# Performance work log

Measured on AMD Instinct MI355X. Metric: run time of the kernel, lower is better.

Reference implementation:

```python
import jax, jax.numpy as jnp
import numpy as np

N = 4096        # n_nodes
IN = 512        # in_features
HEADS = 8       # n_heads
HID = 64        # n_hidden = out_features // n_heads
SLOPE = 0.2     # leaky relu negative slope


def setup_inputs() -> dict:
    key = jax.random.key(0)
    k1, k2, k3, k4 = jax.random.split(key, 4)
    h = jax.random.normal(k1, (N, IN), dtype=jnp.float32)
    W = jax.random.normal(k2, (IN, HEADS * HID), dtype=jnp.float32) * 0.05
    a = jax.random.normal(k3, (2 * HID,), dtype=jnp.float32) * 0.05
    adj = jax.random.uniform(k4, (N, N)) < 0.01
    adj = adj | jnp.eye(N, dtype=bool)
    return {"h": h, "adj_mat": adj[..., None], "W": W, "a": a}


def reference(h, adj_mat, W, a):
    # g[i, h, f] = per-head projected features
    g = (h @ W).reshape(N, HEADS, HID)
    # attention Linear on concat([g_i, g_j]) splits into two dot products
    a_l, a_r = a[:HID], a[HID:]
    el = jnp.einsum('ihf,f->ih', g, a_l)   # score contribution of target i
    er = jnp.einsum('jhf,f->jh', g, a_r)   # score contribution of source j
    e = el[:, None, :] + er[None, :, :]    # [N, N, HEADS]
    e = jnp.where(e >= 0, e, SLOPE * e)    # LeakyReLU
    e = jnp.where(adj_mat, e, -jnp.inf)    # mask non-edges (adj broadcasts over heads)
    attn = jax.nn.softmax(e, axis=1)       # softmax over source nodes j
    out = jnp.einsum('ijh,jhf->ihf', attn, g)
    return out.reshape(N, HEADS * HID)     # is_concat=True
```

## Files before the change

### kernel.cpp

```cpp
#include <hip/hip_runtime.h>
#include <cstdint>
#include <cstddef>

#define N_NODES 4096
#define IN_DIM  512
#define HEADS   8
#define HID     64
#define OUTF    (HEADS * HID)
#define SLOPE   0.2f
#define MAXD    256
#define MAXD2   128

typedef __bf16 bf16_t;
typedef __attribute__((ext_vector_type(8))) __bf16 bf16x8;
typedef __attribute__((ext_vector_type(4))) float    f32x4;

#define GLD16(gp, lp)                                                                  \
    __builtin_amdgcn_global_load_lds((const __attribute__((address_space(1))) void*)(gp), \
                                     (__attribute__((address_space(3))) void*)(lp), 16, 0, 0)

__device__ __forceinline__ unsigned short to_bf16_u(float x) {
    uint32_t u = __builtin_bit_cast(uint32_t, x);
    u += 0x7fffu + ((u >> 16) & 1u);
    return (unsigned short)(u >> 16);
}
__device__ __forceinline__ float bfbits_to_f(unsigned short b) {
    uint32_t u = ((uint32_t)b) << 16;
    return __builtin_bit_cast(float, u);
}

__global__ __launch_bounds__(256) void prep_conv(const float* __restrict__ h,
                                                 unsigned short* __restrict__ hhi,
                                                 const float* __restrict__ W,
                                                 unsigned short* __restrict__ whiT,
                                                 unsigned short* __restrict__ wloT) {
    const int b = blockIdx.x;
    const int tid = threadIdx.x;
    if (b < 2048) {
        const int t = b * 256 + tid;
        const float4 v = ((const float4*)h)[t];
        ushort4 hi;
        hi.x = to_bf16_u(v.x); hi.y = to_bf16_u(v.y);
        hi.z = to_bf16_u(v.z); hi.w = to_bf16_u(v.w);
        ((ushort4*)hhi)[t] = hi;
    } else {
        const int idx = (b - 2048) * 256 + tid;
        const int c   = idx & 511;
        const int kq  = (idx >> 9) * 4;
        ushort4 hv, lv;
        float w0 = W[(size_t)(kq + 0) * OUTF + c];
        float w1 = W[(size_t)(kq + 1) * OUTF + c];
        float w2 = W[(size_t)(kq + 2) * OUTF + c];
        float w3 = W[(size_t)(kq + 3) * OUTF + c];
        hv.x = to_bf16_u(w0); lv.x = to_bf16_u(w0 - bfbits_to_f(hv.x));
        hv.y = to_bf16_u(w1); lv.y = to_bf16_u(w1 - bfbits_to_f(hv.y));
        hv.z = to_bf16_u(w2); lv.z = to_bf16_u(w2 - bfbits_to_f(hv.z));
        hv.w = to_bf16_u(w3); lv.w = to_bf16_u(w3 - bfbits_to_f(hv.w));
        *(ushort4*)&whiT[(size_t)c * IN_DIM + kq] = hv;
        *(ushort4*)&wloT[(size_t)c * IN_DIM + kq] = lv;
    }
}

__global__ __launch_bounds__(256) void gemm_pack(const bf16_t* __restrict__ Ahi,
                                                 const bf16_t* __restrict__ BhiT,
                                                 const bf16_t* __restrict__ BloT,
                                                 const float* __restrict__ a,
                                                 unsigned short* __restrict__ Gb,
                                                 float* __restrict__ el,
                                                 float* __restrict__ er,
                                                 const int* __restrict__ adj,
                                                 unsigned short* __restrict__ bm16) {
    __shared__ bf16_t As[2][64 * 32];
    __shared__ bf16_t Bh[2][64 * 32];
    __shared__ bf16_t Bl[2][64 * 32];
    __shared__ float  elp[2][64], erp[2][64];

    const int tid = threadIdx.x;

    if (blockIdx.x >= 512) {
        const int t = (blockIdx.x - 512) * 256 + tid;
        const int4* src = (const int4*)adj + (size_t)t * 4;
        const int4 v0 = src[0], v1 = src[1], v2 = src[2], v3 = src[3];
        uint32_t m = 0;
        m |= (v0.x != 0) ? 1u << 0 : 0;  m |= (v0.y != 0) ? 1u << 1 : 0;
        m |= (v0.z != 0) ? 1u << 2 : 0;  m |= (v0.w != 0) ? 1u << 3 : 0;
        m |= (v1.x != 0) ? 1u << 4 : 0;  m |= (v1.y != 0) ? 1u << 5 : 0;
        m |= (v1.z != 0) ? 1u << 6 : 0;  m |= (v1.w != 0) ? 1u << 7 : 0;
        m |= (v2.x != 0) ? 1u << 8 : 0;  m |= (v2.y != 0) ? 1u << 9 : 0;
        m |= (v2.z != 0) ? 1u << 10 : 0; m |= (v2.w != 0) ? 1u << 11 : 0;
        m |= (v3.x != 0) ? 1u << 12 : 0; m |= (v3.y != 0) ? 1u << 13 : 0;
        m |= (v3.z != 0) ? 1u << 14 : 0; m |= (v3.w != 0) ? 1u << 15 : 0;
        bm16[t] = (unsigned short)m;
        return;
    }

    const int wid = tid >> 6;
    const int lane = tid & 63;
    const int head = blockIdx.x & 7;
    const int i0 = (blockIdx.x >> 3) * 64;
    const int j0 = head * 64;
    const int l15 = lane & 15, kq = lane >> 4;

    const int srow = tid >> 2;
    const int sc   = (tid & 3) ^ ((srow >> 1) & 3);
    const size_t aoff = (size_t)(i0 + srow) * IN_DIM + sc * 8;
    const size_t boff = (size_t)(j0 + srow) * IN_DIM + sc * 8;

    const int wm = wid >> 1, wn = wid & 1;
    int aro[2], bro[2];
#pragma unroll
    for (int m = 0; m < 2; ++m) {
        const int row = wm * 32 + m * 16 + l15;
        aro[m] = row * 32 + (kq ^ ((row >> 1) & 3)) * 8;
    }
#pragma unroll
    for (int n = 0; n < 2; ++n) {
        const int col = wn * 32 + n * 16 + l15;
        bro[n] = col * 32 + (kq ^ ((col >> 1) & 3)) * 8;
    }

    f32x4 acc[2][2] = {};

    auto stage = [&](int buf, int t) {
        const size_t k0 = (size_t)t * 32;
        GLD16(Ahi  + aoff + k0, &As[buf][tid * 8]);
        GLD16(BhiT + boff + k0, &Bh[buf][tid * 8]);
        GLD16(BloT + boff + k0, &Bl[buf][tid * 8]);
    };

    stage(0, 0);
    for (int t = 0; t < 16; ++t) {
        const int cur = t & 1;
        if (t < 15) {
            stage(cur ^ 1, t + 1);
            asm volatile("s_waitcnt vmcnt(3)" ::: "memory");
        } else {
            asm volatile("s_waitcnt vmcnt(0)" ::: "memory");
        }
        __builtin_amdgcn_s_barrier();
        asm volatile("" ::: "memory");

        bf16x8 af[2], bhf[2], blf[2];
#pragma unroll
        for (int m = 0; m < 2; ++m) af[m] = *(const bf16x8*)&As[cur][aro[m]];
#pragma unroll
        for (int n = 0; n < 2; ++n) bhf[n] = *(const bf16x8*)&Bh[cur][bro[n]];
#pragma unroll
        for (int n = 0; n < 2; ++n) blf[n] = *(const bf16x8*)&Bl[cur][bro[n]];
#pragma unroll
        for (int m = 0; m < 2; ++m)
#pragma unroll
            for (int n = 0; n < 2; ++n) {
                acc[m][n] = __builtin_amdgcn_mfma_f32_16x16x32_bf16(af[m], bhf[n], acc[m][n], 0, 0, 0);
                acc[m][n] = __builtin_amdgcn_mfma_f32_16x16x32_bf16(af[m], blf[n], acc[m][n], 0, 0, 0);
            }

        __builtin_amdgcn_s_barrier();
        asm volatile("" ::: "memory");
    }

#pragma unroll
    for (int m = 0; m < 2; ++m)
#pragma unroll
        for (int n = 0; n < 2; ++n) {
            const int col = j0 + wn * 32 + n * 16 + l15;
#pragma unroll
            for (int q = 0; q < 4; ++q) {
                const int row = i0 + wm * 32 + m * 16 + kq * 4 + q;
                Gb[(size_t)row * OUTF + col] = to_bf16_u(acc[m][n][q]);
            }
        }

    float al[2], arr[2];
#pragma unroll
    for (int n = 0; n < 2; ++n) {
        al[n]  = a[wn * 32 + n * 16 + l15];
        arr[n] = a[64 + wn * 32 + n * 16 + l15];
    }
#pragma unroll
    for (int m = 0; m < 2; ++m)
#pragma unroll
        for (int q = 0; q < 4; ++q) {
            float pe = 0.f, pr = 0.f;
#pragma unroll
            for (int n = 0; n < 2; ++n) {
                const float v = acc[m][n][q];
                pe = fmaf(v, al[n], pe);
                pr = fmaf(v, arr[n], pr);
            }
#pragma unroll
            for (int off = 1; off < 16; off <<= 1) {
                pe += __shfl_xor(pe, off);
                pr += __shfl_xor(pr, off);
            }
            if (l15 == 0) {
                const int lrow = wm * 32 + m * 16 + kq * 4 + q;
                elp[wn][lrow] = pe;
                erp[wn][lrow] = pr;
            }
        }
    __syncthreads();
    if (tid < 64) {
        el[(size_t)(i0 + tid) * HEADS + head] = elp[0][tid] + elp[1][tid];
        er[(size_t)(i0 + tid) * HEADS + head] = erp[0][tid] + erp[1][tid];
    }
}

__global__ __launch_bounds__(512) void gat_attn_wave(const unsigned long long* __restrict__ bm64,
                                                     const unsigned short* __restrict__ Gb,
                                                     const float* __restrict__ el,
                                                     const float* __restrict__ er,
                                                     float* __restrict__ out) {
    __shared__ float pw[8][8][MAXD2 + 8];
    __shared__ int   nbr[8][MAXD2];
    const int tid = threadIdx.x;
    const int lane = tid & 63;
    const int wid = tid >> 6;
    const int i = blockIdx.x * 8 + wid;

    unsigned long long q = bm64[(size_t)i * 64 + lane];
    const int c = __popcll(q);
    int inc = c;
#pragma unroll
    for (int off = 1; off < 64; off <<= 1) {
        const int t = __shfl_up(inc, off);
        if (lane >= off) inc += t;
    }
    const int deg = min(__shfl(inc, 63), MAXD2);
    int pos = inc - c;
    while (q) {
        const int b = __builtin_ctzll(q);
        q &= q - 1;
        if (pos < MAXD2) nbr[wid][pos] = lane * 64 + b;
        ++pos;
    }
    asm volatile("s_waitcnt lgkmcnt(0)" ::: "memory");
    __builtin_amdgcn_wave_barrier();

    const float4 el_lo = *(const float4*)(el + (size_t)i * 8);
    const float4 el_hi = *(const float4*)(el + (size_t)i * 8 + 4);
    float mx[8];
#pragma unroll
    for (int h = 0; h < 8; ++h) mx[h] = -1e30f;
    for (int j = lane; j < deg; j += 64) {
        const int nj = nbr[wid][j];
        const float4 er_lo = *(const float4*)(er + (size_t)nj * 8);
        const float4 er_hi = *(const float4*)(er + (size_t)nj * 8 + 4);
        float e[8] = {el_lo.x + er_lo.x, el_lo.y + er_lo.y, el_lo.z + er_lo.z, el_lo.w + er_lo.w,
                      el_hi.x + er_hi.x, el_hi.y + er_hi.y, el_hi.z + er_hi.z, el_hi.w + er_hi.w};
#pragma unroll
        for (int h = 0; h < 8; ++h) {
            e[h] = (e[h] >= 0.f) ? e[h] : SLOPE * e[h];
            pw[wid][h][j] = e[h];
            mx[h] = fmaxf(mx[h], e[h]);
        }
    }
#pragma unroll
    for (int off = 1; off < 64; off <<= 1)
#pragma unroll
        for (int h = 0; h < 8; ++h) mx[h] = fmaxf(mx[h], __shfl_xor(mx[h], off));

    float s8[8] = {};
    for (int j = lane; j < deg; j += 64) {
#pragma unroll
        for (int h = 0; h < 8; ++h) {
            const float pe = __expf(pw[wid][h][j] - mx[h]);
            pw[wid][h][j] = pe;
            s8[h] += pe;
        }
    }
#pragma unroll
    for (int off = 1; off < 64; off <<= 1)
#pragma unroll
        for (int h = 0; h < 8; ++h) s8[h] += __shfl_xor(s8[h], off);
    asm volatile("s_waitcnt lgkmcnt(0)" ::: "memory");
    __builtin_amdgcn_wave_barrier();

    const int myhead = lane >> 3;
    float sv = s8[0];
    sv = (myhead == 1) ? s8[1] : sv;
    sv = (myhead == 2) ? s8[2] : sv;
    sv = (myhead == 3) ? s8[3] : sv;
    sv = (myhead == 4) ? s8[4] : sv;
    sv = (myhead == 5) ? s8[5] : sv;
    sv = (myhead == 6) ? s8[6] : sv;
    sv = (myhead == 7) ? s8[7] : sv;
    const float inv = 1.f / sv;

    float a8[8] = {};
    const unsigned short* gl = Gb + lane * 8;
#pragma unroll 2
    for (int j = 0; j < deg; ++j) {
        const int nj = nbr[wid][j];
        const float w = pw[wid][myhead][j];
        const uint4 v = *(const uint4*)(gl + (size_t)nj * OUTF);
        a8[0] = fmaf(w, bfbits_to_f((unsigned short)(v.x & 0xffffu)), a8[0]);
        a8[1] = fmaf(w, bfbits_to_f((unsigned short)(v.x >> 16)),     a8[1]);
        a8[2] = fmaf(w, bfbits_to_f((unsigned short)(v.y & 0xffffu)), a8[2]);
        a8[3] = fmaf(w, bfbits_to_f((unsigned short)(v.y >> 16)),     a8[3]);
        a8[4] = fmaf(w, bfbits_to_f((unsigned short)(v.z & 0xffffu)), a8[4]);
        a8[5] = fmaf(w, bfbits_to_f((unsigned short)(v.z >> 16)),     a8[5]);
        a8[6] = fmaf(w, bfbits_to_f((unsigned short)(v.w & 0xffffu)), a8[6]);
        a8[7] = fmaf(w, bfbits_to_f((unsigned short)(v.w >> 16)),     a8[7]);
    }
    float4 o0 = {a8[0] * inv, a8[1] * inv, a8[2] * inv, a8[3] * inv};
    float4 o1 = {a8[4] * inv, a8[5] * inv, a8[6] * inv, a8[7] * inv};
    *(float4*)(out + (size_t)i * OUTF + lane * 8)     = o0;
    *(float4*)(out + (size_t)i * OUTF + lane * 8 + 4) = o1;
}

__global__ __launch_bounds__(256) void gemm_f32(const float* __restrict__ A,
                                                const float* __restrict__ B,
                                                float* __restrict__ C) {
    __shared__ float As[16][68];
    __shared__ float Bs[16][64];
    const int tid = threadIdx.x;
    const int tx = tid & 15, ty = tid >> 4;
    const int i0 = blockIdx.y * 64;
    const int j0 = blockIdx.x * 64;
    const int ar = tid >> 2;
    const int ac = (tid & 3) << 2;
    const int bk = tid >> 4;
    const int bc = (tid & 15) << 2;
    float acc[4][4] = {};
    for (int k0 = 0; k0 < IN_DIM; k0 += 16) {
        const float4 av = *(const float4*)(A + (size_t)(i0 + ar) * IN_DIM + k0 + ac);
        const float4 bv = *(const float4*)(B + (size_t)(k0 + bk) * OUTF + j0 + bc);
        __syncthreads();
        As[ac + 0][ar] = av.x; As[ac + 1][ar] = av.y;
        As[ac + 2][ar] = av.z; As[ac + 3][ar] = av.w;
        *(float4*)&Bs[bk][bc] = bv;
        __syncthreads();
#pragma unroll
        for (int k = 0; k < 16; ++k) {
            const float4 a4 = *(const float4*)&As[k][ty << 2];
            const float4 b4 = *(const float4*)&Bs[k][tx << 2];
            const float am[4] = {a4.x, a4.y, a4.z, a4.w};
            const float bn[4] = {b4.x, b4.y, b4.z, b4.w};
#pragma unroll
            for (int m = 0; m < 4; ++m)
#pragma unroll
                for (int n = 0; n < 4; ++n)
                    acc[m][n] = fmaf(am[m], bn[n], acc[m][n]);
        }
    }
#pragma unroll
    for (int m = 0; m < 4; ++m) {
        float4 v = {acc[m][0], acc[m][1], acc[m][2], acc[m][3]};
        *(float4*)(C + (size_t)(i0 + (ty << 2) + m) * OUTF + j0 + (tx << 2)) = v;
    }
}

__global__ __launch_bounds__(512) void el_er_kernel(const float* __restrict__ g,
                                                    const float* __restrict__ a,
                                                    float* __restrict__ el,
                                                    float* __restrict__ er) {
    const int i = blockIdx.x;
    const int wid = threadIdx.x >> 6;
    const int lane = threadIdx.x & 63;
    const float v = g[(size_t)i * OUTF + wid * HID + lane];
    float pl = v * a[lane];
    float pr = v * a[HID + lane];
#pragma unroll
    for (int off = 1; off < 64; off <<= 1) {
        pl += __shfl_xor(pl, off);
        pr += __shfl_xor(pr, off);
    }
    if (lane == 0) {
        el[(size_t)i * HEADS + wid] = pl;
        er[(size_t)i * HEADS + wid] = pr;
    }
}

__global__ __launch_bounds__(512) void gat_attn_f32(const int* __restrict__ adj,
                                                    const float* __restrict__ g,
                                                    const float* __restrict__ el,
                                                    const float* __restrict__ er,
                                                    float* __restrict__ out) {
    const int i = blockIdx.x;
    const int tid = threadIdx.x;
    const int lane = tid & 63;
    const int wid = tid >> 6;

    __shared__ int   nbr[MAXD];
    __shared__ float p[HEADS][MAXD + 2];
    __shared__ float red[8][256];
    __shared__ float sinv[8];
    __shared__ int   wave_base[8];
    __shared__ int   s_deg;

    const int4* row = (const int4*)(adj + (size_t)i * N_NODES);
    const int4 w0 = row[tid * 2 + 0];
    const int4 w1 = row[tid * 2 + 1];
    uint32_t msk = 0;
    if (w0.x) msk |= 1u;   if (w0.y) msk |= 2u;
    if (w0.z) msk |= 4u;   if (w0.w) msk |= 8u;
    if (w1.x) msk |= 16u;  if (w1.y) msk |= 32u;
    if (w1.z) msk |= 64u;  if (w1.w) msk |= 128u;

    const int c = __popc(msk);
    int inc = c;
#pragma unroll
    for (int off = 1; off < 64; off <<= 1) {
        const int t = __shfl_up(inc, off);
        if (lane >= off) inc += t;
    }
    if (lane == 63) wave_base[wid] = inc;
    __syncthreads();
    if (tid == 0) {
        int run = 0;
#pragma unroll
        for (int w = 0; w < 8; ++w) { const int t = wave_base[w]; wave_base[w] = run; run += t; }
        s_deg = run;
    }
    __syncthreads();
    int pos = wave_base[wid] + inc - c;
#pragma unroll
    for (int b = 0; b < 8; ++b) {
        if (msk & (1u << b)) {
            if (pos < MAXD) nbr[pos] = tid * 8 + b;
            ++pos;
        }
    }
    __syncthreads();
    const int deg = min(s_deg, MAXD);

    const float eli = el[(size_t)i * HEADS + wid];
    float m = -1e30f;
    for (int j = lane; j < deg; j += 64) {
        float e = eli + er[(size_t)nbr[j] * HEADS + wid];
        e = (e >= 0.f) ? e : SLOPE * e;
        p[wid][j] = e;
        m = fmaxf(m, e);
    }
#pragma unroll
    for (int off = 1; off < 64; off <<= 1) m = fmaxf(m, __shfl_xor(m, off));
    float s = 0.f;
    for (int j = lane; j < deg; j += 64) {
        const float pe = __expf(p[wid][j] - m);
        p[wid][j] = pe;
        s += pe;
    }
#pragma unroll
    for (int off = 1; off < 64; off <<= 1) s += __shfl_xor(s, off);
    if (lane == 0) sinv[wid] = 1.f / s;
    __syncthreads();

    const int half = wid >> 2, jslot = wid & 3;
    const int head = half * 4 + (lane >> 4);
    const int f4 = (lane & 15) * 4;
    const float* gbase = g + (size_t)head * HID + f4;
    float4 acc = {0.f, 0.f, 0.f, 0.f};
#pragma unroll 4
    for (int j = jslot; j < deg; j += 4) {
        const int nj = nbr[j];
        const float w = p[head][j];
        const float4 v = *(const float4*)(gbase + (size_t)nj * OUTF);
        acc.x = fmaf(w, v.x, acc.x);
        acc.y = fmaf(w, v.y, acc.y);
        acc.z = fmaf(w, v.z, acc.z);
        acc.w = fmaf(w, v.w, acc.w);
    }
    *(float4*)&red[wid][(lane >> 4) * 64 + f4] = acc;
    __syncthreads();

    const int hf = tid >> 8, loc = tid & 255;
    const float v = red[hf * 4 + 0][loc] + red[hf * 4 + 1][loc] +
                    red[hf * 4 + 2][loc] + red[hf * 4 + 3][loc];
    out[(size_t)i * OUTF + tid] = v * sinv[tid >> 6];
}

extern "C" void kernel_launch(void* const* d_in, const int* in_sizes, int n_in,
                              void* d_out, int out_size, void* d_ws, size_t ws_size,
                              hipStream_t stream) {
    const float* h   = (const float*)d_in[0];
    const int*   adj = (const int*)d_in[1];
    const float* W   = (const float*)d_in[2];
    const float* a   = (const float*)d_in[3];
    float* out = (float*)d_out;
    char* ws = (char*)d_ws;

    const size_t G_OFF   = 0;
    const size_t EL_OFF  = 8388608;
    const size_t ER_OFF  = 8519680;
    const size_t BM_OFF  = 8650752;
    const size_t HHI_OFF = 10747904;
    const size_t WHI_OFF = 14942208;
    const size_t WLO_OFF = 15466496;
    const size_t NEED_FULL = 15990784;

    float* el = (float*)(ws + EL_OFF);
    float* er = (float*)(ws + ER_OFF);

    if (ws_size >= NEED_FULL) {
        unsigned short* gbf  = (unsigned short*)(ws + G_OFF);
        unsigned short* bm   = (unsigned short*)(ws + BM_OFF);
        unsigned short* hhi  = (unsigned short*)(ws + HHI_OFF);
        unsigned short* whiT = (unsigned short*)(ws + WHI_OFF);
        unsigned short* wloT = (unsigned short*)(ws + WLO_OFF);
        prep_conv<<<2304, 256, 0, stream>>>(h, hhi, W, whiT, wloT);
        gemm_pack<<<4608, 256, 0, stream>>>((const bf16_t*)hhi, (const bf16_t*)whiT,
                                            (const bf16_t*)wloT, a, gbf, el, er, adj, bm);
        gat_attn_wave<<<512, 512, 0, stream>>>((const unsigned long long*)bm, gbf, el, er, out);
    } else {
        float* g = (float*)(ws + G_OFF);
        gemm_f32<<<dim3(8, 64), 256, 0, stream>>>(h, W, g);
        el_er_kernel<<<N_NODES, 512, 0, stream>>>(g, a, el, er);
        gat_attn_f32<<<N_NODES, 512, 0, stream>>>(adj, g, el, er, out);
    }
}
```

Measured before the change: 49.08 us.

## Split each attention row across two waves and double GEMM K-tile

The GEMM K tile grows from 32 to 64 with a new 8-way XOR swizzle, halving the number of pipeline iterations and barriers. The attention kernel now assigns two waves per node: each computes softmax for four heads and half the neighbour gather, and partial sums are reduced through shared memory before a block-wide store. This doubles the number of waves launched for the latency-bound gather. It costs more LDS per block and adds __syncthreads calls where the old code used only wave-level sync.

```diff
diff --git a/kernel.cpp b/kernel.cpp
--- a/kernel.cpp
+++ b/kernel.cpp
@@ -70,9 +70,9 @@
                                                  float* __restrict__ er,
                                                  const int* __restrict__ adj,
                                                  unsigned short* __restrict__ bm16) {
-    __shared__ bf16_t As[2][64 * 32];
-    __shared__ bf16_t Bh[2][64 * 32];
-    __shared__ bf16_t Bl[2][64 * 32];
+    __shared__ bf16_t As[2][64 * 64];
+    __shared__ bf16_t Bh[2][64 * 64];
+    __shared__ bf16_t Bl[2][64 * 64];
     __shared__ float  elp[2][64], erp[2][64];
 
     const int tid = threadIdx.x;
@@ -101,59 +101,74 @@
     const int j0 = head * 64;
     const int l15 = lane & 15, kq = lane >> 4;
 
-    const int srow = tid >> 2;
-    const int sc   = (tid & 3) ^ ((srow >> 1) & 3);
-    const size_t aoff = (size_t)(i0 + srow) * IN_DIM + sc * 8;
-    const size_t boff = (size_t)(j0 + srow) * IN_DIM + sc * 8;
+    const int sr0 = wid * 16 + (lane >> 3);
+    const int sc  = (lane & 7) ^ (sr0 & 7);
+    const size_t aoff = (size_t)(i0 + sr0) * IN_DIM + sc * 8;
+    const size_t boff = (size_t)(j0 + sr0) * IN_DIM + sc * 8;
+    const int ld0 = wid * 1024 + lane * 8;
 
     const int wm = wid >> 1, wn = wid & 1;
-    int aro[2], bro[2];
+    int aro[2][2], bro[2][2];
 #pragma unroll
     for (int m = 0; m < 2; ++m) {
         const int row = wm * 32 + m * 16 + l15;
-        aro[m] = row * 32 + (kq ^ ((row >> 1) & 3)) * 8;
+#pragma unroll
+        for (int ks = 0; ks < 2; ++ks)
+            aro[m][ks] = row * 64 + (((ks * 4 + kq) ^ (row & 7)) * 8);
     }
 #pragma unroll
     for (int n = 0; n < 2; ++n) {
         const int col = wn * 32 + n * 16 + l15;
-        bro[n] = col * 32 + (kq ^ ((col >> 1) & 3)) * 8;
+#pragma unroll
+        for (int ks = 0; ks < 2; ++ks)
+            bro[n][ks] = col * 64 + (((ks * 4 + kq) ^ (col & 7)) * 8);
     }
 
     f32x4 acc[2][2] = {};
 
     auto stage = [&](int buf, int t) {
-        const size_t k0 = (size_t)t * 32;
-        GLD16(Ahi  + aoff + k0, &As[buf][tid * 8]);
-        GLD16(BhiT + boff + k0, &Bh[buf][tid * 8]);
-        GLD16(BloT + boff + k0, &Bl[buf][tid * 8]);
+        const size_t k0 = (size_t)t * 64;
+        GLD16(Ahi  + aoff + k0,                       &As[buf][ld0]);
+        GLD16(Ahi  + aoff + (size_t)8 * IN_DIM + k0,  &As[buf][ld0 + 512]);
+        GLD16(BhiT + boff + k0,                       &Bh[buf][ld0]);
+        GLD16(BhiT + boff + (size_t)8 * IN_DIM + k0,  &Bh[buf][ld0 + 512]);
+        GLD16(BloT + boff + k0,                       &Bl[buf][ld0]);
+        GLD16(BloT + boff + (size_t)8 * IN_DIM + k0,  &Bl[buf][ld0 + 512]);
     };
 
     stage(0, 0);
-    for (int t = 0; t < 16; ++t) {
+    for (int t = 0; t < 8; ++t) {
         const int cur = t & 1;
-        if (t < 15) {
+        if (t < 7) {
             stage(cur ^ 1, t + 1);
-            asm volatile("s_waitcnt vmcnt(3)" ::: "memory");
+            asm volatile("s_waitcnt vmcnt(6)" ::: "memory");
         } else {
             asm volatile("s_waitcnt vmcnt(0)" ::: "memory");
         }
         __builtin_amdgcn_s_barrier();
         asm volatile("" ::: "memory");
 
-        bf16x8 af[2], bhf[2], blf[2];
-#pragma unroll
-        for (int m = 0; m < 2; ++m) af[m] = *(const bf16x8*)&As[cur][aro[m]];
-#pragma unroll
-        for (int n = 0; n < 2; ++n) bhf[n] = *(const bf16x8*)&Bh[cur][bro[n]];
-#pragma unroll
-        for (int n = 0; n < 2; ++n) blf[n] = *(const bf16x8*)&Bl[cur][bro[n]];
+        bf16x8 af[2][2], bh2[2][2], bl2[2][2];
 #pragma unroll
         for (int m = 0; m < 2; ++m)
 #pragma unroll
-            for (int n = 0; n < 2; ++n) {
-                acc[m][n] = __builtin_amdgcn_mfma_f32_16x16x32_bf16(af[m], bhf[n], acc[m][n], 0, 0, 0);
-                acc[m][n] = __builtin_amdgcn_mfma_f32_16x16x32_bf16(af[m], blf[n], acc[m][n], 0, 0, 0);
+            for (int ks = 0; ks < 2; ++ks) af[m][ks] = *(const bf16x8*)&As[cur][aro[m][ks]];
+#pragma unroll
+        for (int n = 0; n < 2; ++n)
+#pragma unroll
+            for (int ks = 0; ks < 2; ++ks) {
+                bh2[n][ks] = *(const bf16x8*)&Bh[cur][bro[n][ks]];
+                bl2[n][ks] = *(const bf16x8*)&Bl[cur][bro[n][ks]];
             }
+#pragma unroll
+        for (int ks = 0; ks < 2; ++ks)
+#pragma unroll
+            for (int m = 0; m < 2; ++m)
+#pragma unroll
+                for (int n = 0; n < 2; ++n) {
+                    acc[m][n] = __builtin_amdgcn_mfma_f32_16x16x32_bf16(af[m][ks], bh2[n][ks], acc[m][n], 0, 0, 0);
+                    acc[m][n] = __builtin_amdgcn_mfma_f32_16x16x32_bf16(af[m][ks], bl2[n][ks], acc[m][n], 0, 0, 0);
+                }
 
         __builtin_amdgcn_s_barrier();
         asm volatile("" ::: "memory");
@@ -211,12 +226,15 @@
                                                      const float* __restrict__ el,
                                                      const float* __restrict__ er,
                                                      float* __restrict__ out) {
-    __shared__ float pw[8][8][MAXD2 + 8];
-    __shared__ int   nbr[8][MAXD2];
+    __shared__ int   nbr[4][2][MAXD2];
+    __shared__ float pw[4][8][MAXD2 + 8];
+    __shared__ float red[4][2][OUTF];
+    __shared__ float sinv[4][8];
     const int tid = threadIdx.x;
     const int lane = tid & 63;
     const int wid = tid >> 6;
-    const int i = blockIdx.x * 8 + wid;
+    const int r = wid >> 1, sub = wid & 1;
+    const int i = blockIdx.x * 4 + r;
 
     unsigned long long q = bm64[(size_t)i * 64 + lane];
     const int c = __popcll(q);
@@ -231,68 +249,56 @@
     while (q) {
         const int b = __builtin_ctzll(q);
         q &= q - 1;
-        if (pos < MAXD2) nbr[wid][pos] = lane * 64 + b;
+        if (pos < MAXD2) nbr[r][sub][pos] = lane * 64 + b;
         ++pos;
     }
     asm volatile("s_waitcnt lgkmcnt(0)" ::: "memory");
     __builtin_amdgcn_wave_barrier();
 
-    const float4 el_lo = *(const float4*)(el + (size_t)i * 8);
-    const float4 el_hi = *(const float4*)(el + (size_t)i * 8 + 4);
-    float mx[8];
-#pragma unroll
-    for (int h = 0; h < 8; ++h) mx[h] = -1e30f;
+    const float4 el4 = *(const float4*)(el + (size_t)i * 8 + sub * 4);
+    float mx[4] = {-1e30f, -1e30f, -1e30f, -1e30f};
     for (int j = lane; j < deg; j += 64) {
-        const int nj = nbr[wid][j];
-        const float4 er_lo = *(const float4*)(er + (size_t)nj * 8);
-        const float4 er_hi = *(const float4*)(er + (size_t)nj * 8 + 4);
-        float e[8] = {el_lo.x + er_lo.x, el_lo.y + er_lo.y, el_lo.z + er_lo.z, el_lo.w + er_lo.w,
-                      el_hi.x + er_hi.x, el_hi.y + er_hi.y, el_hi.z + er_hi.z, el_hi.w + er_hi.w};
-#pragma unroll
-        for (int h = 0; h < 8; ++h) {
-            e[h] = (e[h] >= 0.f) ? e[h] : SLOPE * e[h];
-            pw[wid][h][j] = e[h];
-            mx[h] = fmaxf(mx[h], e[h]);
+        const int nj = nbr[r][sub][j];
+        const float4 er4 = *(const float4*)(er + (size_t)nj * 8 + sub * 4);
+        float e[4] = {el4.x + er4.x, el4.y + er4.y, el4.z + er4.z, el4.w + er4.w};
+#pragma unroll
+        for (int hh = 0; hh < 4; ++hh) {
+            e[hh] = (e[hh] >= 0.f) ? e[hh] : SLOPE * e[hh];
+            pw[r][sub * 4 + hh][j] = e[hh];
+            mx[hh] = fmaxf(mx[hh], e[hh]);
         }
     }
 #pragma unroll
     for (int off = 1; off < 64; off <<= 1)
 #pragma unroll
-        for (int h = 0; h < 8; ++h) mx[h] = fmaxf(mx[h], __shfl_xor(mx[h], off));
-
-    float s8[8] = {};
+        for (int hh = 0; hh < 4; ++hh) mx[hh] = fmaxf(mx[hh], __shfl_xor(mx[hh], off));
+
+    float s4[4] = {};
     for (int j = lane; j < deg; j += 64) {
 #pragma unroll
-        for (int h = 0; h < 8; ++h) {
-            const float pe = __expf(pw[wid][h][j] - mx[h]);
-            pw[wid][h][j] = pe;
-            s8[h] += pe;
+        for (int hh = 0; hh < 4; ++hh) {
+            const float pe = __expf(pw[r][sub * 4 + hh][j] - mx[hh]);
+            pw[r][sub * 4 + hh][j] = pe;
+            s4[hh] += pe;
         }
     }
 #pragma unroll
     for (int off = 1; off < 64; off <<= 1)
 #pragma unroll
-        for (int h = 0; h < 8; ++h) s8[h] += __shfl_xor(s8[h], off);
-    asm volatile("s_waitcnt lgkmcnt(0)" ::: "memory");
-    __builtin_amdgcn_wave_barrier();
+        for (int hh = 0; hh < 4; ++hh) s4[hh] += __shfl_xor(s4[hh], off);
+    if (lane == 0) {
+#pragma unroll
+        for (int hh = 0; hh < 4; ++hh) sinv[r][sub * 4 + hh] = 1.f / s4[hh];
+    }
+    __syncthreads();
 
     const int myhead = lane >> 3;
-    float sv = s8[0];
-    sv = (myhead == 1) ? s8[1] : sv;
-    sv = (myhead == 2) ? s8[2] : sv;
-    sv = (myhead == 3) ? s8[3] : sv;
-    sv = (myhead == 4) ? s8[4] : sv;
-    sv = (myhead == 5) ? s8[5] : sv;
-    sv = (myhead == 6) ? s8[6] : sv;
-    sv = (myhead == 7) ? s8[7] : sv;
-    const float inv = 1.f / sv;
-
     float a8[8] = {};
     const unsigned short* gl = Gb + lane * 8;
-#pragma unroll 2
-    for (int j = 0; j < deg; ++j) {
-        const int nj = nbr[wid][j];
-        const float w = pw[wid][myhead][j];
+#pragma unroll 4
+    for (int j = sub; j < deg; j += 2) {
+        const int nj = nbr[r][sub][j];
+        const float w = pw[r][myhead][j];
         const uint4 v = *(const uint4*)(gl + (size_t)nj * OUTF);
         a8[0] = fmaf(w, bfbits_to_f((unsigned short)(v.x & 0xffffu)), a8[0]);
         a8[1] = fmaf(w, bfbits_to_f((unsigned short)(v.x >> 16)),     a8[1]);
@@ -303,10 +309,17 @@
         a8[6] = fmaf(w, bfbits_to_f((unsigned short)(v.w & 0xffffu)), a8[6]);
         a8[7] = fmaf(w, bfbits_to_f((unsigned short)(v.w >> 16)),     a8[7]);
     }
-    float4 o0 = {a8[0] * inv, a8[1] * inv, a8[2] * inv, a8[3] * inv};
-    float4 o1 = {a8[4] * inv, a8[5] * inv, a8[6] * inv, a8[7] * inv};
-    *(float4*)(out + (size_t)i * OUTF + lane * 8)     = o0;
-    *(float4*)(out + (size_t)i * OUTF + lane * 8 + 4) = o1;
+    float4 lo = {a8[0], a8[1], a8[2], a8[3]};
+    float4 hi = {a8[4], a8[5], a8[6], a8[7]};
+    *(float4*)&red[r][sub][lane * 8 + 0] = lo;
+    *(float4*)&red[r][sub][lane * 8 + 4] = hi;
+    __syncthreads();
+
+#pragma unroll
+    for (int rr = 0; rr < 4; ++rr) {
+        const float v = red[rr][0][tid] + red[rr][1][tid];
+        out[(size_t)(blockIdx.x * 4 + rr) * OUTF + tid] = v * sinv[rr][tid >> 6];
+    }
 }
 
 __global__ __launch_bounds__(256) void gemm_f32(const float* __restrict__ A,
@@ -501,7 +514,7 @@
         prep_conv<<<2304, 256, 0, stream>>>(h, hhi, W, whiT, wloT);
         gemm_pack<<<4608, 256, 0, stream>>>((const bf16_t*)hhi, (const bf16_t*)whiT,
                                             (const bf16_t*)wloT, a, gbf, el, er, adj, bm);
-        gat_attn_wave<<<512, 512, 0, stream>>>((const unsigned long long*)bm, gbf, el, er, out);
+        gat_attn_wave<<<1024, 512, 0, stream>>>((const unsigned long long*)bm, gbf, el, er, out);
     } else {
         float* g = (float*)(ws + G_OFF);
         gemm_f32<<<dim3(8, 64), 256, 0, stream>>>(h, W, g);
```

Result: faster. 43.91 us (-10.5%).
